# Kernel tuning notes

Hardware: AMD Instinct MI355X
Metric: run time of the kernel (lower is better)

Reference implementation:

```python
import jax, jax.numpy as jnp
import numpy as np

N_NODES = 50000
N_EDGES = 800000
NUM_GRAPHS = 128
FEAT = 128
HID = 64
NUM_LAYERS = 3
OUT = 2
K = 30
LATENT = HID * NUM_LAYERS + 1  # 193 = conv1 kernel size & stride


def _lin(k, i, o):
    s = 1.0 / np.sqrt(i)
    return jax.random.uniform(k, (i, o), jnp.float32, -s, s)


def setup_inputs() -> dict:
    key = jax.random.key(0)
    ks = jax.random.split(key, 16)
    x = jax.random.normal(ks[0], (N_NODES, FEAT), jnp.float32)
    edge_index = jax.random.randint(ks[1], (2, N_EDGES), 0, N_NODES, dtype=jnp.int64)
    batch = jnp.sort(jax.random.randint(ks[2], (N_NODES,), 0, NUM_GRAPHS, dtype=jnp.int64))
    w0 = _lin(ks[3], FEAT, HID); b0 = jnp.zeros((HID,), jnp.float32)
    w1 = _lin(ks[4], HID, HID);  b1 = jnp.zeros((HID,), jnp.float32)
    w2 = _lin(ks[5], HID, HID);  b2 = jnp.zeros((HID,), jnp.float32)
    w3 = _lin(ks[6], HID, 1);    b3 = jnp.zeros((1,), jnp.float32)
    conv1_w = jax.random.normal(ks[7], (16, 1, LATENT), jnp.float32) * (1.0 / np.sqrt(LATENT))
    conv1_b = jnp.zeros((16,), jnp.float32)
    conv2_w = jax.random.normal(ks[8], (32, 16, 5), jnp.float32) * (1.0 / np.sqrt(16 * 5))
    conv2_b = jnp.zeros((32,), jnp.float32)
    dense_dim = (int((K - 2) / 2 + 1) - 5 + 1) * 32  # 352
    lin1_w = _lin(ks[9], dense_dim, 256); lin1_b = jnp.zeros((256,), jnp.float32)
    lin2_w = _lin(ks[10], 256, OUT);      lin2_b = jnp.zeros((OUT,), jnp.float32)
    return dict(x=x, edge_index=edge_index, batch=batch,
                w0=w0, b0=b0, w1=w1, b1=b1, w2=w2, b2=b2, w3=w3, b3=b3,
                conv1_w=conv1_w, conv1_b=conv1_b, conv2_w=conv2_w, conv2_b=conv2_b,
                lin1_w=lin1_w, lin1_b=lin1_b, lin2_w=lin2_w, lin2_b=lin2_b)


def _gcn(h_in, w, b, src, dst, norm, n):
    # GCNConv: out_i = sum_j d_i^-1/2 d_j^-1/2 (x_j W) over A+I, plus bias
    h = h_in @ w
    msg = h[src] * norm[:, None]  # gather over edges (incl. self loops)
    return jax.ops.segment_sum(msg, dst, num_segments=n) + b


def _sort_pool(x, batch, k, g):
    # per-graph descending sort on last channel, top-k, zero-pad
    n, d = x.shape
    order = jnp.lexsort((-x[:, -1], batch))  # primary: batch asc, secondary: last feat desc
    xs, bs = x[order], batch[order]
    counts = jax.ops.segment_sum(jnp.ones((n,), jnp.int32), batch, num_segments=g)
    starts = jnp.cumsum(counts) - counts
    rank = jnp.arange(n) - starts[bs]
    slot = jnp.where(rank < k, rank, k)  # overflow nodes dumped in slot k (discarded)
    out = jnp.zeros((g, k + 1, d), x.dtype).at[bs, slot].set(xs)
    return out[:, :k].reshape(g, k * d)


def _conv1d(z, w, stride):
    return jax.lax.conv_general_dilated(z, w, window_strides=(stride,), padding='VALID',
                                        dimension_numbers=('NCH', 'OIH', 'NCH'))


def reference(x, edge_index, batch, w0, b0, w1, b1, w2, b2, w3, b3,
              conv1_w, conv1_b, conv2_w, conv2_b, lin1_w, lin1_b, lin2_w, lin2_b):
    n = x.shape[0]
    loop = jnp.arange(n, dtype=edge_index.dtype)
    src = jnp.concatenate([edge_index[0], loop])
    dst = jnp.concatenate([edge_index[1], loop])
    deg = jax.ops.segment_sum(jnp.ones_like(src, jnp.float32), dst, num_segments=n)
    dinv = jnp.where(deg > 0, jax.lax.rsqrt(deg), 0.0)
    norm = dinv[src] * dinv[dst]

    h1 = jnp.tanh(_gcn(x,  w0, b0, src, dst, norm, n))
    h2 = jnp.tanh(_gcn(h1, w1, b1, src, dst, norm, n))
    h3 = jnp.tanh(_gcn(h2, w2, b2, src, dst, norm, n))
    h4 = jnp.tanh(_gcn(h3, w3, b3, src, dst, norm, n))
    hcat = jnp.concatenate([h1, h2, h3, h4], axis=-1)  # [N, 193]

    p = _sort_pool(hcat, batch, K, NUM_GRAPHS)  # [G, K*193]
    z = p[:, None, :]                                   # [G, 1, K*193]
    z = jax.nn.relu(_conv1d(z, conv1_w, LATENT) + conv1_b[None, :, None])  # [G,16,K]
    g, c, l = z.shape
    z = z.reshape(g, c, l // 2, 2).max(axis=-1)         # MaxPool1d(2,2) -> [G,16,15]
    z = jax.nn.relu(_conv1d(z, conv2_w, 1) + conv2_b[None, :, None])       # [G,32,11]
    z = z.reshape(g, -1)                                # [G,352]
    z = jax.nn.relu(z @ lin1_w + lin1_b)
    # dropout is identity in eval mode
    return z @ lin2_w + lin2_b
```

## Files before the change

kernel.cpp:

```cpp
#include <hip/hip_runtime.h>
#include <math.h>

#define NGRAPH 128
#define KTOP 30
#define LATENT 193
#define HID 64

typedef unsigned short u16;

__global__ void k_zero(int* edeg, int n) {
    int i = blockIdx.x * blockDim.x + threadIdx.x;
    if (i < n) edeg[i] = 0;
}

template <bool SCALE>
__device__ __forceinline__ void gemm_tile(const float* __restrict__ A,
                                          const float* __restrict__ W,
                                          const float* __restrict__ dinv,
                                          float* __restrict__ Hs,
                                          int M, int K, int br,
                                          float (*As)[68], float (*Bs)[68]) {
    int tid = threadIdx.x;
    int tx = tid & 15, ty = tid >> 4;
    int kA = (tid & 7) * 4;
    int rA = tid >> 3;
    int kB = tid >> 3;
    int cB = (tid & 7) * 8;
    float c[4][4] = {};
    for (int k0 = 0; k0 < K; k0 += 32) {
#pragma unroll
        for (int it = 0; it < 2; ++it) {
            int row = it * 32 + rA;
            int grow = br + row;
            float4 v = make_float4(0.f, 0.f, 0.f, 0.f);
            if (grow < M) v = *(const float4*)(A + (size_t)grow * K + k0 + kA);
            As[kA + 0][row] = v.x;
            As[kA + 1][row] = v.y;
            As[kA + 2][row] = v.z;
            As[kA + 3][row] = v.w;
        }
        {
            const float* wp = W + (size_t)(k0 + kB) * 64 + cB;
            float4 v0 = *(const float4*)(wp);
            float4 v1 = *(const float4*)(wp + 4);
            *(float4*)&Bs[kB][cB] = v0;
            *(float4*)&Bs[kB][cB + 4] = v1;
        }
        __syncthreads();
#pragma unroll
        for (int kk = 0; kk < 32; ++kk) {
            float4 a4 = *(const float4*)&As[kk][ty * 4];
            float4 b4 = *(const float4*)&Bs[kk][tx * 4];
            c[0][0] += a4.x * b4.x; c[0][1] += a4.x * b4.y; c[0][2] += a4.x * b4.z; c[0][3] += a4.x * b4.w;
            c[1][0] += a4.y * b4.x; c[1][1] += a4.y * b4.y; c[1][2] += a4.y * b4.z; c[1][3] += a4.y * b4.w;
            c[2][0] += a4.z * b4.x; c[2][1] += a4.z * b4.y; c[2][2] += a4.z * b4.z; c[2][3] += a4.z * b4.w;
            c[3][0] += a4.w * b4.x; c[3][1] += a4.w * b4.y; c[3][2] += a4.w * b4.z; c[3][3] += a4.w * b4.w;
        }
        __syncthreads();
    }
#pragma unroll
    for (int i = 0; i < 4; i++) {
        int row = br + ty * 4 + i;
        if (row >= M) continue;
        float d = SCALE ? dinv[row] : 1.f;
        float4 o;
        o.x = c[i][0] * d; o.y = c[i][1] * d; o.z = c[i][2] * d; o.w = c[i][3] * d;
        *(float4*)(Hs + (size_t)row * HID + tx * 4) = o;
    }
}

__global__ __launch_bounds__(256) void k_gemm_hist(
        const float* __restrict__ A, const float* __restrict__ W,
        float* __restrict__ Hs, int M, int K, int NG,
        const int* __restrict__ dst, const int* __restrict__ batch,
        int* edeg, u16* __restrict__ rank, int* starts,
        int E, int n, int NH) {
    __shared__ float As[32][68];
    __shared__ float Bs[32][68];
    int bid = blockIdx.x;
    if ((bid & 1) == 0) {
        int gid = bid >> 1;
        if (gid >= NG) return;
        gemm_tile<false>(A, W, nullptr, Hs, M, K, gid * 64, As, Bs);
    } else {
        int fid = bid >> 1;
        if (fid >= NH) return;
        int t = threadIdx.x;
        int gi = fid * 256 + t;
        if (gi < n) {
            int b = batch[gi];
            if (gi == 0) {
                for (int g = 0; g <= b; g++) starts[g] = 0;
            } else {
                int pb = batch[gi - 1];
                for (int g = pb + 1; g <= b; g++) starts[g] = gi;
            }
            if (gi == n - 1) {
                for (int g = b + 1; g <= NGRAPH; g++) starts[g] = n;
            }
        }
        int base = fid * 1024;
#pragma unroll
        for (int k = 0; k < 4; k++) {
            int e = base + k * 256 + t;
            if (e < E) {
                int d = dst[e];
                rank[e] = (u16)atomicAdd(&edeg[d], 1);
            }
        }
    }
}

__global__ void k_scan1(const int* __restrict__ edeg, int* offs, int* bsum,
                        float* dinv, int n) {
    __shared__ int s[256];
    int t = threadIdx.x;
    int gi = blockIdx.x * 256 + t;
    int v = (gi < n) ? edeg[gi] : 0;
    if (gi < n) dinv[gi] = rsqrtf((float)(v + 1));
    s[t] = v;
    __syncthreads();
    for (int o = 1; o < 256; o <<= 1) {
        int add = (t >= o) ? s[t - o] : 0;
        __syncthreads();
        s[t] += add;
        __syncthreads();
    }
    if (gi < n) offs[gi] = s[t] - v;
    if (t == 255) bsum[blockIdx.x] = s[255];
}

__global__ void k_scan23(int* offs, const int* __restrict__ bsum,
                         int n, int E, int nb) {
    __shared__ int s[256];
    int t = threadIdx.x;
    int bid = blockIdx.x;
    int v = (t < nb) ? bsum[t] : 0;
    s[t] = v;
    __syncthreads();
    for (int o = 1; o < 256; o <<= 1) {
        int add = (t >= o) ? s[t - o] : 0;
        __syncthreads();
        s[t] += add;
        __syncthreads();
    }
    int boffv = (bid == 0) ? 0 : s[bid - 1];
    int gi = bid * 256 + t;
    if (gi < n) offs[gi] += boffv;
    if (gi == 0) offs[n] = E;
}

__global__ __launch_bounds__(256) void k_fill(const int* __restrict__ src,
                                              const int* __restrict__ dst,
                                              const u16* __restrict__ rank,
                                              const int* __restrict__ offs,
                                              u16* __restrict__ csr, int E) {
    int t = blockIdx.x * 256 + threadIdx.x;
    int e0 = t * 4;
    if (e0 + 4 <= E) {
        int4 s4 = *(const int4*)(src + e0);
        int4 d4 = *(const int4*)(dst + e0);
        uint2 rv = *(const uint2*)(rank + e0);
        csr[offs[d4.x] + (rv.x & 0xffff)] = (u16)s4.x;
        csr[offs[d4.y] + (rv.x >> 16)]    = (u16)s4.y;
        csr[offs[d4.z] + (rv.y & 0xffff)] = (u16)s4.z;
        csr[offs[d4.w] + (rv.y >> 16)]    = (u16)s4.w;
    } else {
        for (int e = e0; e < E; e++)
            csr[offs[dst[e]] + rank[e]] = (u16)src[e];
    }
}

__global__ __launch_bounds__(256) void k_gemm(const float* __restrict__ A,
                                              const float* __restrict__ W,
                                              const float* __restrict__ dinv,
                                              float* __restrict__ Hs,
                                              int M, int K) {
    __shared__ float As[32][68];
    __shared__ float Bs[32][68];
    gemm_tile<true>(A, W, dinv, Hs, M, K, blockIdx.x * 64, As, Bs);
}

template <bool DEFER, bool FUSE_TS>
__global__ __launch_bounds__(256) void k_agg(const float* __restrict__ Hs,
                                             const u16* __restrict__ csr,
                                             const int* __restrict__ offs,
                                             const float* __restrict__ dinv,
                                             const float* __restrict__ b,
                                             float* __restrict__ H, int n,
                                             const float* __restrict__ w3,
                                             float* __restrict__ ts) {
    int wid = threadIdx.x >> 6;
    int lane = threadIdx.x & 63;
    int node = blockIdx.x * 4 + wid;
    if (node >= n) return;
    float d = dinv[node];
    float acc = Hs[(size_t)node * HID + lane];
    if (DEFER) acc *= d;
    int s0 = offs[node], e1 = offs[node + 1];
    int mid = s0 + ((e1 - s0) >> 1);
    int iA = s0, iB = mid;
    while (iA + 8 <= mid && iB + 8 <= e1) {
        float pa = 0.f, pb = 0.f;
#pragma unroll
        for (int k = 0; k < 8; k++) {
            int uA = csr[iA + k];
            int uB = csr[iB + k];
            float vA = Hs[(size_t)uA * HID + lane];
            float vB = Hs[(size_t)uB * HID + lane];
            if (DEFER) { vA *= dinv[uA]; vB *= dinv[uB]; }
            pa += vA; pb += vB;
        }
        acc += pa + pb;
        iA += 8; iB += 8;
    }
    for (; iA + 8 <= mid; iA += 8) {
        float pa = 0.f;
#pragma unroll
        for (int k = 0; k < 8; k++) {
            int u = csr[iA + k];
            float v = Hs[(size_t)u * HID + lane];
            if (DEFER) v *= dinv[u];
            pa += v;
        }
        acc += pa;
    }
    for (; iA < mid; ++iA) {
        int u = csr[iA];
        float v = Hs[(size_t)u * HID + lane];
        if (DEFER) v *= dinv[u];
        acc += v;
    }
    for (; iB + 8 <= e1; iB += 8) {
        float pb = 0.f;
#pragma unroll
        for (int k = 0; k < 8; k++) {
            int u = csr[iB + k];
            float v = Hs[(size_t)u * HID + lane];
            if (DEFER) v *= dinv[u];
            pb += v;
        }
        acc += pb;
    }
    for (; iB < e1; ++iB) {
        int u = csr[iB];
        float v = Hs[(size_t)u * HID + lane];
        if (DEFER) v *= dinv[u];
        acc += v;
    }
    float h = tanhf(acc * d + b[lane]);
    H[(size_t)node * HID + lane] = h;
    if (FUSE_TS) {
        float v = h * w3[lane];
        for (int o = 32; o > 0; o >>= 1) v += __shfl_down(v, o, 64);
        if (lane == 0) ts[node] = v * d;
    }
}

__global__ __launch_bounds__(1024) void k_select_tail(
        const float* __restrict__ h1, const float* __restrict__ h2,
        const float* __restrict__ h3, const float* __restrict__ ts,
        const u16* __restrict__ csr, const int* __restrict__ offs,
        const float* __restrict__ dinv, const float* __restrict__ b3,
        const int* __restrict__ starts,
        const float* __restrict__ c1w, const float* __restrict__ c1b,
        const float* __restrict__ c2w, const float* __restrict__ c2b,
        const float* __restrict__ l1w, const float* __restrict__ l1b,
        const float* __restrict__ l2w, const float* __restrict__ l2b,
        float* __restrict__ out) {
    __shared__ float p[KTOP * LATENT];
    __shared__ float w1s[16 * LATENT];
    __shared__ float w2s[32 * 16 * 5];
    __shared__ float vv[2048];
    __shared__ int   pr[2048];
    __shared__ int   sel_s[KTOP];
    __shared__ float zpart[960];
    __shared__ float z1[16 * KTOP];
    __shared__ float z1p[16 * 15];
    __shared__ float flat[352];
    __shared__ float part[1024];
    __shared__ float y1[256];
    int g = blockIdx.x;
    int t = threadIdx.x;
    int s = starts[g];
    int c = starts[g + 1] - s;
    if (c > 2048) c = 2048;

    for (int i = t; i < 16 * LATENT; i += 1024) w1s[i] = c1w[i];
    for (int i = t; i < 32 * 16 * 5; i += 1024) w2s[i] = c2w[i];
    if (t < KTOP) sel_s[t] = -1;

    float bb = b3[0];
    for (int i = t; i < c; i += 1024) {
        int node = s + i;
        float acc = ts[node];
        int es = offs[node], ee = offs[node + 1];
        for (int j = es; j < ee; j++) acc += ts[csr[j]];
        vv[i] = tanhf(acc * dinv[node] + bb);
    }
    __syncthreads();

    int chalf = c >> 1;
    for (int i2 = t; i2 < 2 * c; i2 += 1024) {
        int i = i2 >> 1, half = i2 & 1;
        float vi = vv[i];
        int j0 = half ? chalf : 0;
        int j1 = half ? c : chalf;
        int r = 0;
        for (int j = j0; j < j1; j++) {
            float vj = vv[j];
            r += (vj > vi) || (vj == vi && j < i);
        }
        pr[i2] = r;
    }
    __syncthreads();
    for (int i = t; i < c; i += 1024) {
        int r = pr[2 * i] + pr[2 * i + 1];
        if (r < KTOP) sel_s[r] = s + i;
    }
    __syncthreads();

    for (int i = t; i < KTOP * LATENT; i += 1024) {
        int slot = i / LATENT;
        int j = i - slot * LATENT;
        int node = sel_s[slot];
        float v = 0.f;
        if (node >= 0) {
            if (j < 64)       v = h1[(size_t)node * HID + j];
            else if (j < 128) v = h2[(size_t)node * HID + j - 64];
            else if (j < 192) v = h3[(size_t)node * HID + j - 128];
            else              v = vv[node - s];
        }
        p[i] = v;
    }
    __syncthreads();
    if (t < 960) {
        int to = (t < 480) ? t : t - 480;
        int half = (t < 480) ? 0 : 1;
        int ch = to / KTOP, tt = to - ch * KTOP;
        const float* wp = &w1s[ch * LATENT];
        const float* pp = &p[tt * LATENT];
        int j0 = half ? 96 : 0;
        int j1 = half ? LATENT : 96;
        float sa = 0.f;
        for (int j = j0; j < j1; j++) sa += pp[j] * wp[j];
        zpart[t] = sa;
    }
    __syncthreads();
    if (t < 480) {
        int ch = t / KTOP, tt = t - ch * KTOP;
        z1[ch * KTOP + tt] = fmaxf(zpart[t] + zpart[480 + t] + c1b[ch], 0.f);
    }
    __syncthreads();
    if (t < 16 * 15) {
        int ch = t / 15, tt = t - ch * 15;
        z1p[t] = fmaxf(z1[ch * KTOP + 2 * tt], z1[ch * KTOP + 2 * tt + 1]);
    }
    __syncthreads();
    if (t < 32 * 11) {
        int c2 = t / 11, tt = t - c2 * 11;
        float sa = c2b[c2];
        for (int c1i = 0; c1i < 16; c1i++) {
            const float* wp = &w2s[(c2 * 16 + c1i) * 5];
            const float* zp = &z1p[c1i * 15 + tt];
#pragma unroll
            for (int dt = 0; dt < 5; dt++) sa += zp[dt] * wp[dt];
        }
        flat[c2 * 11 + tt] = fmaxf(sa, 0.f);
    }
    __syncthreads();
    {
        int o = t & 255, ch = t >> 8;
        int i0 = ch * 88, i1 = i0 + 88;
        float sa = 0.f;
        for (int i = i0; i < i1; i++) sa += flat[i] * l1w[(size_t)i * 256 + o];
        part[t] = sa;
    }
    __syncthreads();
    if (t < 256)
        y1[t] = fmaxf(part[t] + part[256 + t] + part[512 + t] + part[768 + t] + l1b[t], 0.f);
    __syncthreads();
    if (t < 128) {
        int o = t >> 6, lane = t & 63;
        float sa = 0.f;
        for (int i = lane; i < 256; i += 64) sa += y1[i] * l2w[(size_t)i * 2 + o];
        for (int off = 32; off > 0; off >>= 1) sa += __shfl_down(sa, off, 64);
        if (lane == 0) out[g * 2 + o] = sa + l2b[o];
    }
}

static inline char* align256(char* p) {
    return (char*)(((uintptr_t)p + 255) & ~(uintptr_t)255);
}

extern "C" void kernel_launch(void* const* d_in, const int* in_sizes, int n_in,
                              void* d_out, int out_size, void* d_ws, size_t ws_size,
                              hipStream_t stream) {
    const float* x     = (const float*)d_in[0];
    const int*  eidx   = (const int*)d_in[1];
    const int*  batch  = (const int*)d_in[2];
    const float* w0    = (const float*)d_in[3];
    const float* b0    = (const float*)d_in[4];
    const float* w1    = (const float*)d_in[5];
    const float* b1    = (const float*)d_in[6];
    const float* w2    = (const float*)d_in[7];
    const float* b2    = (const float*)d_in[8];
    const float* w3    = (const float*)d_in[9];
    const float* b3    = (const float*)d_in[10];
    const float* c1w   = (const float*)d_in[11];
    const float* c1b   = (const float*)d_in[12];
    const float* c2w   = (const float*)d_in[13];
    const float* c2b   = (const float*)d_in[14];
    const float* l1w   = (const float*)d_in[15];
    const float* l1b   = (const float*)d_in[16];
    const float* l2w   = (const float*)d_in[17];
    const float* l2b   = (const float*)d_in[18];

    int N = in_sizes[2];
    int E = in_sizes[1] / 2;
    int K0 = in_sizes[0] / N;
    const int* esrc = eidx;
    const int* edst = eidx + E;

    char* w = (char*)d_ws;
    float* dinv  = (float*)w;             w = align256(w + (size_t)N * 4);
    int*   edeg  = (int*)w;               w = align256(w + (size_t)N * 4);
    int*   offs  = (int*)w;               w = align256(w + (size_t)(N + 1) * 4);
    int*   bsum  = (int*)w;               w = align256(w + 1024);
    float* ts    = (float*)w;             w = align256(w + (size_t)N * 4);
    int* starts  = (int*)w;               w = align256(w + (NGRAPH + 1) * 4);
    u16* rank    = (u16*)w;               w = align256(w + (size_t)E * 2);
    u16* csr     = (u16*)w;               w = align256(w + (size_t)E * 2);
    float* Hs    = (float*)w;             w = align256(w + (size_t)N * HID * 4);
    float* h1    = (float*)w;             w = align256(w + (size_t)N * HID * 4);
    float* h2    = (float*)w;             w = align256(w + (size_t)N * HID * 4);
    float* h3    = (float*)w;             w = align256(w + (size_t)N * HID * 4);

    int nb = (N + 255) / 256;
    int NG = (N + 63) / 64;
    int NH = (E + 1023) / 1024;
    int agg_grid = (N + 3) / 4;

    k_zero<<<nb, 256, 0, stream>>>(edeg, N);

    int g1 = 2 * (NG > NH ? NG : NH);
    k_gemm_hist<<<g1, 256, 0, stream>>>(x, w0, Hs, N, K0, NG,
                                        edst, batch, edeg, rank, starts, E, N, NH);

    k_scan1<<<nb, 256, 0, stream>>>(edeg, offs, bsum, dinv, N);
    k_scan23<<<nb, 256, 0, stream>>>(offs, bsum, N, E, nb);

    k_fill<<<(E / 4 + 255) / 256 + 1, 256, 0, stream>>>(esrc, edst, rank, offs, csr, E);

    k_agg<true, false><<<agg_grid, 256, 0, stream>>>(Hs, csr, offs, dinv, b0, h1, N, nullptr, nullptr);
    k_gemm<<<NG, 256, 0, stream>>>(h1, w1, dinv, Hs, N, HID);
    k_agg<false, false><<<agg_grid, 256, 0, stream>>>(Hs, csr, offs, dinv, b1, h2, N, nullptr, nullptr);
    k_gemm<<<NG, 256, 0, stream>>>(h2, w2, dinv, Hs, N, HID);
    k_agg<false, true><<<agg_grid, 256, 0, stream>>>(Hs, csr, offs, dinv, b2, h3, N, w3, ts);

    k_select_tail<<<NGRAPH, 1024, 0, stream>>>(h1, h2, h3, ts, csr, offs, dinv, b3,
                                               starts,
                                               c1w, c1b, c2w, c2b,
                                               l1w, l1b, l2w, l2b,
                                               (float*)d_out);
}
```

Measured before the change: 282.8 us.

## Split aggregation into two feature-half passes with two edges per wavefront

The aggregation kernel becomes two launches, each covering 32 of the 64 features. The two 32-lane halves of a wavefront handle alternating edges, and their sums are combined with a cross-half shuffle. The aim is to shrink each pass's gather working set (half the feature columns) to improve cache hit rates. In exchange, the CSR index and dinv reads are doubled, there are extra launches, and the fused ts output now depends on a read-modify-write across the two launches.

```diff
diff --git a/kernel.cpp b/kernel.cpp
--- a/kernel.cpp
+++ b/kernel.cpp
@@ -181,79 +181,58 @@
     gemm_tile<true>(A, W, dinv, Hs, M, K, blockIdx.x * 64, As, Bs);
 }
 
-template <bool DEFER, bool FUSE_TS>
-__global__ __launch_bounds__(256) void k_agg(const float* __restrict__ Hs,
-                                             const u16* __restrict__ csr,
-                                             const int* __restrict__ offs,
-                                             const float* __restrict__ dinv,
-                                             const float* __restrict__ b,
-                                             float* __restrict__ H, int n,
-                                             const float* __restrict__ w3,
-                                             float* __restrict__ ts) {
+template <bool DEFER, bool FUSE_TS, int HALF>
+__global__ __launch_bounds__(256) void k_agg_half(
+        const float* __restrict__ Hs, const u16* __restrict__ csr,
+        const int* __restrict__ offs, const float* __restrict__ dinv,
+        const float* __restrict__ b, float* __restrict__ H, int n,
+        const float* __restrict__ w3, float* __restrict__ ts) {
     int wid = threadIdx.x >> 6;
     int lane = threadIdx.x & 63;
+    int feat = (lane & 31) + HALF * 32;
+    int slot = lane >> 5;
     int node = blockIdx.x * 4 + wid;
     if (node >= n) return;
     float d = dinv[node];
-    float acc = Hs[(size_t)node * HID + lane];
-    if (DEFER) acc *= d;
-    int s0 = offs[node], e1 = offs[node + 1];
-    int mid = s0 + ((e1 - s0) >> 1);
-    int iA = s0, iB = mid;
-    while (iA + 8 <= mid && iB + 8 <= e1) {
-        float pa = 0.f, pb = 0.f;
+    float acc = 0.f;
+    if (slot == 0) {
+        acc = Hs[(size_t)node * HID + feat];
+        if (DEFER) acc *= d;
+    }
+    int s = offs[node], e = offs[node + 1];
+    int base = s;
+    while (base + 16 <= e) {
+        float p = 0.f;
 #pragma unroll
         for (int k = 0; k < 8; k++) {
-            int uA = csr[iA + k];
-            int uB = csr[iB + k];
-            float vA = Hs[(size_t)uA * HID + lane];
-            float vB = Hs[(size_t)uB * HID + lane];
-            if (DEFER) { vA *= dinv[uA]; vB *= dinv[uB]; }
-            pa += vA; pb += vB;
-        }
-        acc += pa + pb;
-        iA += 8; iB += 8;
-    }
-    for (; iA + 8 <= mid; iA += 8) {
-        float pa = 0.f;
-#pragma unroll
-        for (int k = 0; k < 8; k++) {
-            int u = csr[iA + k];
-            float v = Hs[(size_t)u * HID + lane];
+            int u = csr[base + 2 * k + slot];
+            float v = Hs[(size_t)u * HID + feat];
             if (DEFER) v *= dinv[u];
-            pa += v;
-        }
-        acc += pa;
-    }
-    for (; iA < mid; ++iA) {
-        int u = csr[iA];
-        float v = Hs[(size_t)u * HID + lane];
-        if (DEFER) v *= dinv[u];
-        acc += v;
-    }
-    for (; iB + 8 <= e1; iB += 8) {
-        float pb = 0.f;
-#pragma unroll
-        for (int k = 0; k < 8; k++) {
-            int u = csr[iB + k];
-            float v = Hs[(size_t)u * HID + lane];
+            p += v;
+        }
+        acc += p;
+        base += 16;
+    }
+    for (; base < e; base += 2) {
+        int pos = base + slot;
+        if (pos < e) {
+            int u = csr[pos];
+            float v = Hs[(size_t)u * HID + feat];
             if (DEFER) v *= dinv[u];
-            pb += v;
-        }
-        acc += pb;
-    }
-    for (; iB < e1; ++iB) {
-        int u = csr[iB];
-        float v = Hs[(size_t)u * HID + lane];
-        if (DEFER) v *= dinv[u];
-        acc += v;
-    }
-    float h = tanhf(acc * d + b[lane]);
-    H[(size_t)node * HID + lane] = h;
+            acc += v;
+        }
+    }
+    acc += __shfl_xor(acc, 32, 64);
+    float h = tanhf(acc * d + b[feat]);
+    if (slot == 0) H[(size_t)node * HID + feat] = h;
     if (FUSE_TS) {
-        float v = h * w3[lane];
-        for (int o = 32; o > 0; o >>= 1) v += __shfl_down(v, o, 64);
-        if (lane == 0) ts[node] = v * d;
+        float v = h * w3[feat];
+        for (int o = 16; o > 0; o >>= 1) v += __shfl_down(v, o, 32);
+        if (lane == 0) {
+            float part = v * d;
+            if (HALF == 0) ts[node] = part;
+            else           ts[node] += part;
+        }
     }
 }
 
@@ -452,11 +431,14 @@
 
     k_fill<<<(E / 4 + 255) / 256 + 1, 256, 0, stream>>>(esrc, edst, rank, offs, csr, E);
 
-    k_agg<true, false><<<agg_grid, 256, 0, stream>>>(Hs, csr, offs, dinv, b0, h1, N, nullptr, nullptr);
+    k_agg_half<true, false, 0><<<agg_grid, 256, 0, stream>>>(Hs, csr, offs, dinv, b0, h1, N, nullptr, nullptr);
+    k_agg_half<true, false, 1><<<agg_grid, 256, 0, stream>>>(Hs, csr, offs, dinv, b0, h1, N, nullptr, nullptr);
     k_gemm<<<NG, 256, 0, stream>>>(h1, w1, dinv, Hs, N, HID);
-    k_agg<false, false><<<agg_grid, 256, 0, stream>>>(Hs, csr, offs, dinv, b1, h2, N, nullptr, nullptr);
+    k_agg_half<false, false, 0><<<agg_grid, 256, 0, stream>>>(Hs, csr, offs, dinv, b1, h2, N, nullptr, nullptr);
+    k_agg_half<false, false, 1><<<agg_grid, 256, 0, stream>>>(Hs, csr, offs, dinv, b1, h2, N, nullptr, nullptr);
     k_gemm<<<NG, 256, 0, stream>>>(h2, w2, dinv, Hs, N, HID);
-    k_agg<false, true><<<agg_grid, 256, 0, stream>>>(Hs, csr, offs, dinv, b2, h3, N, w3, ts);
+    k_agg_half<false, true, 0><<<agg_grid, 256, 0, stream>>>(Hs, csr, offs, dinv, b2, h3, N, w3, ts);
+    k_agg_half<false, true, 1><<<agg_grid, 256, 0, stream>>>(Hs, csr, offs, dinv, b2, h3, N, w3, ts);
 
     k_select_tail<<<NGRAPH, 1024, 0, stream>>>(h1, h2, h3, ts, csr, offs, dinv, b3,
                                                starts,
```

After: 334.3 us. 18.2% more time.
